# Kernel tuning notes

Hardware: AMD Instinct MI355X
Metric: run time of the kernel (lower is better)

The kernel has to match this reference:

```python
import math
import jax, jax.numpy as jnp
import numpy as np

H, N2, B, L = 256, 32, 8, 4096
DT_MIN, DT_MAX = 1e-3, 1e-1

def setup_inputs() -> dict:
    key = jax.random.key(0)
    ks = jax.random.split(key, 6)
    u = jax.random.normal(ks[0], (B, H, L), dtype=jnp.float32)
    # log_dt uniform in [log(dt_min), log(dt_max)] as in S4DKernel.__init__
    log_dt = jax.random.uniform(ks[1], (H,), dtype=jnp.float32) * (
        math.log(DT_MAX) - math.log(DT_MIN)) + math.log(DT_MIN)
    C = jax.random.normal(ks[2], (H, N2, 2), dtype=jnp.float32)  # view_as_real of complex C
    log_A_real = jnp.log(0.5 * jnp.ones((H, N2), dtype=jnp.float32))
    A_imag = math.pi * jnp.broadcast_to(jnp.arange(N2, dtype=jnp.float32), (H, N2))
    D = jax.random.normal(ks[3], (H,), dtype=jnp.float32)
    W = jax.random.normal(ks[4], (2 * H, H), dtype=jnp.float32) / math.sqrt(H)
    b = jax.random.normal(ks[5], (2 * H,), dtype=jnp.float32) * 0.01
    return {"u": u, "log_dt": log_dt, "C": C, "log_A_real": log_A_real,
            "A_imag": A_imag, "D": D, "W": W, "b": b}

def reference(u, log_dt, C, log_A_real, A_imag, D, W, b):
    # ---- S4DKernel: generate convolution kernel k (H, L) ----
    Lk = u.shape[-1]
    dt = jnp.exp(log_dt)                                  # (H,)
    Cc = C[..., 0] + 1j * C[..., 1]                       # (H, N2) complex
    A = -jnp.exp(log_A_real) + 1j * A_imag                # (H, N2) complex
    dtA = A * dt[:, None]                                 # (H, N2)
    # Vandermonde: exp(dtA * l) for l in [0, L)  -> (H, N2, L) complex
    K = jnp.exp(dtA[:, :, None] * jnp.arange(Lk, dtype=jnp.float32))
    Ct = Cc * (jnp.exp(dtA) - 1.0) / A                    # (H, N2)
    k = 2.0 * jnp.einsum('hn,hnl->hl', Ct, K).real        # (H, L) float32
    # ---- FFT long convolution ----
    n = 2 * Lk
    k_f = jnp.fft.rfft(k, n=n)                            # (H, n//2+1)
    u_f = jnp.fft.rfft(u, n=n)                            # (B, H, n//2+1)
    y = jnp.fft.irfft(u_f * k_f, n=n)[..., :Lk]           # (B, H, L)
    y = y + u * D[:, None]                                # skip connection
    y = jax.nn.gelu(y, approximate=False)                 # nn.GELU (exact)
    # ---- output 1x1 conv (H -> 2H) + GLU over channel dim ----
    z = jnp.einsum('oh,bhl->bol', W, y) + b[None, :, None]  # (B, 2H, L)
    a, g = jnp.split(z, 2, axis=1)
    return a * jax.nn.sigmoid(g)                          # (B, H, L)
```

## Files before the change

### kernel.cpp

```cpp
#include <hip/hip_runtime.h>
#include <math.h>

#define H 256
#define N2 32
#define Bsz 8
#define Lseq 4096
#define BH (Bsz*H)
#define NCH 32
#define LC (Lseq/NCH)
#define HN (H*N2)

#define Y_OFF  0
#define WB_OFF (Y_OFF + (BH*Lseq/2))
#define TB_OFF (WB_OFF + (512*256/2))
#define EB_OFF (TB_OFF + (H*128*128/2))
#define VB_OFF (EB_OFF + (H*128*64/2))

typedef __attribute__((ext_vector_type(8))) short bf16x8;
typedef __attribute__((ext_vector_type(8))) unsigned short u16x8;
typedef __attribute__((ext_vector_type(4))) float f32x4;

__device__ __forceinline__ unsigned short f2bf(float x) {
  union { float f; unsigned int u; } v; v.f = x;
  unsigned int r = v.u + 0x7fffu + ((v.u >> 16) & 1u);
  return (unsigned short)(r >> 16);
}
__device__ __forceinline__ unsigned int packbf(float lo, float hi) {
  return (unsigned int)f2bf(lo) | ((unsigned int)f2bf(hi) << 16);
}
__device__ __forceinline__ float bf2f(unsigned short b) {
  union { unsigned int u; float f; } v; v.u = ((unsigned int)b) << 16;
  return v.f;
}

__global__ __launch_bounds__(512) void k_prep(const float* __restrict__ log_dt,
                                              const float* __restrict__ C,
                                              const float* __restrict__ lar,
                                              const float* __restrict__ aim,
                                              const float* __restrict__ W,
                                              unsigned short* __restrict__ Wb,
                                              unsigned short* __restrict__ Tb,
                                              unsigned short* __restrict__ Eb,
                                              unsigned short* __restrict__ Vb) {
  __shared__ float kpart[3][128];
  __shared__ unsigned short kbuf[128];
  int h   = blockIdx.x;
  int tid = threadIdx.x;
  int j   = tid & 127;
  int ng  = tid >> 7;
  if (tid < 128) {
    int i = h * 128 + tid;
    float4 v = *(const float4*)&W[i * 4];
    uint2 p; p.x = packbf(v.x, v.y); p.y = packbf(v.z, v.w);
    *(uint2*)&Wb[i * 4] = p;
  }
  float dt = expf(log_dt[h]);
  float kacc = 0.f;
  unsigned short* Erow = Eb + (h * 128 + j) * 64;
  for (int nn = 0; nn < 8; nn++) {
    int n  = ng * 8 + nn;
    int hn = (h << 5) + n;
    float Ar = -expf(lar[hn]), Ai = aim[hn];
    float dAr = Ar * dt, dAi = Ai * dt;
    float er = expf(dAr), sw, cw;
    sincosf(dAi, &sw, &cw);
    float wr = er * cw, wi = er * sw;
    float emr = wr - 1.f, emi = wi;
    float inv = 1.f / (Ar * Ar + Ai * Ai);
    float qr = (emr * Ar + emi * Ai) * inv;
    float qi = (emi * Ar - emr * Ai) * inv;
    float Cr = C[2 * hn], Ci = C[2 * hn + 1];
    float c2r = 2.f * (Cr * qr - Ci * qi);
    float c2i = 2.f * (Cr * qi + Ci * qr);
    float ej = expf(dAr * (float)j), sj, cj;
    sincosf(dAi * (float)j, &sj, &cj);
    kacc = fmaf(c2r, ej * cj, fmaf(-c2i, ej * sj, kacc));
    float e1 = expf(dAr * (float)(j + 1)), s1, c1;
    sincosf(dAi * (float)(j + 1), &s1, &c1);
    float w1r = e1 * c1, w1i = e1 * s1;
    Erow[2 * n]     = f2bf(c2r * w1r - c2i * w1i);
    Erow[2 * n + 1] = f2bf(-(c2r * w1i + c2i * w1r));
    float ev = expf(dAr * (float)(127 - j)), sv, cv;
    sincosf(dAi * (float)(127 - j), &sv, &cv);
    Vb[(h * 64 + 2 * n) * 128 + j]     = f2bf(ev * cv);
    Vb[(h * 64 + 2 * n + 1) * 128 + j] = f2bf(ev * sv);
  }
  if (ng) kpart[ng - 1][j] = kacc;
  __syncthreads();
  if (ng == 0) kbuf[j] = f2bf(kacc + kpart[0][j] + kpart[1][j] + kpart[2][j]);
  __syncthreads();
  unsigned short* Trow = Tb + (h * 128 + j) * 128;
#pragma unroll
  for (int s8i = 0; s8i < 4; s8i++) {
    int s8 = ng * 4 + s8i;
    u16x8 v;
#pragma unroll
    for (int t = 0; t < 8; t++) {
      int m = s8 * 8 + t;
      v[t] = (j >= m) ? kbuf[j - m] : (unsigned short)0;
    }
    *(u16x8*)&Trow[s8 * 8] = v;
  }
}

__global__ __launch_bounds__(256, 8) void k_ssm(const float* __restrict__ u,
                                             const float* __restrict__ log_dt,
                                             const float* __restrict__ lar,
                                             const float* __restrict__ aim,
                                             const unsigned short* __restrict__ Vb,
                                             const unsigned short* __restrict__ Tb,
                                             const unsigned short* __restrict__ Eb,
                                             const float* __restrict__ Dp,
                                             unsigned short* __restrict__ yb) {
  __shared__ __align__(16) unsigned short Ub[32][136];
  __shared__ __align__(16) float          Fb[32][68];
  int g   = blockIdx.x;
  int h   = g & 255, b = g >> 8;
  int tid = threadIdx.x;
  int wv = tid >> 6, lane = tid & 63;
  int n16 = lane & 15, quad = lane >> 4;
  const float* ubase = u + (b * 256 + h) * 4096;

#pragma unroll
  for (int i = 0; i < 2; i++) {
    int idx = tid * 2 + i;
    float4 va = *(const float4*)(ubase + idx * 8);
    float4 vb4 = *(const float4*)(ubase + idx * 8 + 4);
    unsigned short* dst = &Ub[idx >> 4][(idx & 15) * 8];
    *(unsigned int*)(dst)     = packbf(va.x, va.y);
    *(unsigned int*)(dst + 2) = packbf(va.z, va.w);
    *(unsigned int*)(dst + 4) = packbf(vb4.x, vb4.y);
    *(unsigned int*)(dst + 6) = packbf(vb4.z, vb4.w);
  }
  __syncthreads();

  {
    f32x4 sacc[2] = {};
#pragma unroll
    for (int ks = 0; ks < 128; ks += 32) {
      int kc = ks + quad * 8;
      bf16x8 bv = *(const bf16x8*)&Vb[(h * 64 + wv * 16 + n16) * 128 + kc];
#pragma unroll
      for (int mt = 0; mt < 2; mt++) {
        bf16x8 av = *(const bf16x8*)&Ub[mt * 16 + n16][kc];
        sacc[mt] = __builtin_amdgcn_mfma_f32_16x16x32_bf16(av, bv, sacc[mt], 0, 0, 0);
      }
    }
#pragma unroll
    for (int mt = 0; mt < 2; mt++)
#pragma unroll
      for (int reg = 0; reg < 4; reg++)
        Fb[mt * 16 + quad * 4 + reg][wv * 16 + n16] = sacc[mt][reg];
  }
  __syncthreads();

  if (wv == 0 && lane < 32) {
    int n = lane, hn = (h << 5) + n;
    float dt  = expf(log_dt[h]);
    float dAr = -expf(lar[hn]) * dt, dAi = aim[hn] * dt;
    float eL = expf(dAr * (float)LC), sL, cL;
    sincosf(dAi * (float)LC, &sL, &cL);
    float wLr = eL * cL, wLi = eL * sL;
    float fr = 0.f, fi = 0.f;
    for (int c = 0; c < NCH; c++) {
      float sr = Fb[c][2 * n], si = Fb[c][2 * n + 1];
      __builtin_amdgcn_sched_barrier(0);
      *(unsigned int*)&Fb[c][n] = packbf(fr, fi);
      float nr = fmaf(wLr, fr, fmaf(-wLi, fi, sr));
      float ni = fmaf(wLr, fi, fmaf(wLi, fr, si));
      fr = nr; fi = ni;
    }
  }
  __syncthreads();

  f32x4 acc[2][2] = {};
#pragma unroll
  for (int ksi = 0; ksi < 6; ksi++) {
    int kc = ksi * 32 + quad * 8;
    bf16x8 a2[2];
#pragma unroll
    for (int mt = 0; mt < 2; mt++)
      a2[mt] = (ksi < 4)
                 ? *(const bf16x8*)&Ub[mt * 16 + n16][kc]
                 : *(const bf16x8*)((const unsigned short*)&Fb[mt * 16 + n16][0] + (kc - 128));
#pragma unroll
    for (int ntl = 0; ntl < 2; ntl++) {
      int j = (wv * 2 + ntl) * 16 + n16;
      bf16x8 bv = (ksi < 4) ? *(const bf16x8*)&Tb[(h * 128 + j) * 128 + kc]
                            : *(const bf16x8*)&Eb[(h * 128 + j) * 64 + kc - 128];
#pragma unroll
      for (int mt = 0; mt < 2; mt++)
        acc[mt][ntl] = __builtin_amdgcn_mfma_f32_16x16x32_bf16(a2[mt], bv, acc[mt][ntl], 0, 0, 0);
    }
  }

  float Dh = Dp[h];
  unsigned short* ybase = yb + (b * 256 + h) * 4096;
#pragma unroll
  for (int mt = 0; mt < 2; mt++) {
#pragma unroll
    for (int reg = 0; reg < 4; reg++) {
      int c = mt * 16 + quad * 4 + reg;
#pragma unroll
      for (int ntl = 0; ntl < 2; ntl++) {
        int j = (wv * 2 + ntl) * 16 + n16;
        float uv = bf2f(Ub[c][j]);
        float v  = fmaf(Dh, uv, acc[mt][ntl][reg]);
        float t2 = 1.5957691216057308f * v * fmaf(0.044715f, v * v, 1.0f);
        float ge = v / (1.0f + expf(-t2));
        ybase[c * 128 + j] = f2bf(ge);
      }
    }
  }
}

__global__ __launch_bounds__(256) void k_gemm(const unsigned short* __restrict__ yb,
                                              const unsigned short* __restrict__ Wb,
                                              const float* __restrict__ bias,
                                              float* __restrict__ out) {
  __shared__ unsigned short Ys[2][128][72];
  int tid  = threadIdx.x;
  int l0   = blockIdx.x * 128;
  int o0   = blockIdx.y * 64;
  int bb   = blockIdx.z;
  int wave = tid >> 6;
  int lane = tid & 63;
  int wo   = wave & 1;
  int wl   = wave >> 1;
  int n    = lane & 15;
  int quad = lane >> 4;
  int kcol = tid & 63;
  int lg0  = tid >> 6;

  f32x4 acc_a[2][4] = {};
  f32x4 acc_g[2][4] = {};

  u16x8 yreg[4];
  {
    const unsigned short* yr = yb + (size_t)(bb * 256 + kcol) * 4096 + l0;
#pragma unroll
    for (int i = 0; i < 4; i++)
      yreg[i] = *(const u16x8*)&yr[(lg0 * 4 + i) * 8];
  }

#pragma unroll
  for (int kk = 0; kk < H; kk += 64) {
    int cur = (kk >> 6) & 1;
#pragma unroll
    for (int i = 0; i < 4; i++) {
      int l8 = (lg0 * 4 + i) * 8;
#pragma unroll
      for (int jj = 0; jj < 8; jj++)
        Ys[cur][l8 + jj][kcol] = yreg[i][jj];
    }
    __syncthreads();
    if (kk + 64 < H) {
      const unsigned short* yr = yb + (size_t)(bb * 256 + kk + 64 + kcol) * 4096 + l0;
#pragma unroll
      for (int i = 0; i < 4; i++)
        yreg[i] = *(const u16x8*)&yr[(lg0 * 4 + i) * 8];
    }
#pragma unroll
    for (int ks = 0; ks < 64; ks += 32) {
      int kc = ks + quad * 8;
      bf16x8 af_a[2], af_g[2], bfr[4];
#pragma unroll
      for (int mt = 0; mt < 2; mt++) {
        int oa = o0 + wo * 32 + mt * 16 + n;
        af_a[mt] = *(const bf16x8*)&Wb[(size_t)oa * 256 + kk + kc];
        af_g[mt] = *(const bf16x8*)&Wb[(size_t)(256 + oa) * 256 + kk + kc];
      }
#pragma unroll
      for (int lt = 0; lt < 4; lt++)
        bfr[lt] = *(const bf16x8*)&Ys[cur][wl * 64 + lt * 16 + n][kc];
#pragma unroll
      for (int mt = 0; mt < 2; mt++)
#pragma unroll
        for (int lt = 0; lt < 4; lt++) {
          acc_a[mt][lt] = __builtin_amdgcn_mfma_f32_16x16x32_bf16(af_a[mt], bfr[lt], acc_a[mt][lt], 0, 0, 0);
          acc_g[mt][lt] = __builtin_amdgcn_mfma_f32_16x16x32_bf16(af_g[mt], bfr[lt], acc_g[mt][lt], 0, 0, 0);
        }
    }
  }
#pragma unroll
  for (int mt = 0; mt < 2; mt++) {
    int ob = o0 + wo * 32 + mt * 16 + quad * 4;
#pragma unroll
    for (int reg = 0; reg < 4; reg++) {
      int op = ob + reg;
      float ba = bias[op], bg = bias[H + op];
      float* orow = &out[(bb * H + op) * Lseq + l0 + wl * 64 + n];
#pragma unroll
      for (int lt = 0; lt < 4; lt++) {
        float a = acc_a[mt][lt][reg] + ba;
        float gg = acc_g[mt][lt][reg] + bg;
        orow[lt * 16] = a / (1.0f + expf(-gg));
      }
    }
  }
}

extern "C" void kernel_launch(void* const* d_in, const int* in_sizes, int n_in,
                              void* d_out, int out_size, void* d_ws, size_t ws_size,
                              hipStream_t stream) {
  const float* u      = (const float*)d_in[0];
  const float* log_dt = (const float*)d_in[1];
  const float* C      = (const float*)d_in[2];
  const float* lar    = (const float*)d_in[3];
  const float* aim    = (const float*)d_in[4];
  const float* Dp     = (const float*)d_in[5];
  const float* W      = (const float*)d_in[6];
  const float* bias   = (const float*)d_in[7];
  float* out = (float*)d_out;
  float* ws  = (float*)d_ws;
  unsigned short* yb  = (unsigned short*)(ws + Y_OFF);
  unsigned short* Wb  = (unsigned short*)(ws + WB_OFF);
  unsigned short* Tbg = (unsigned short*)(ws + TB_OFF);
  unsigned short* Ebg = (unsigned short*)(ws + EB_OFF);
  unsigned short* Vbg = (unsigned short*)(ws + VB_OFF);

  hipLaunchKernelGGL(k_prep, dim3(H), dim3(512), 0, stream, log_dt, C, lar, aim, W, Wb, Tbg, Ebg, Vbg);
  hipLaunchKernelGGL(k_ssm,  dim3(BH), dim3(256), 0, stream, u, log_dt, lar, aim, Vbg, Tbg, Ebg, Dp, yb);
  hipLaunchKernelGGL(k_gemm, dim3(Lseq / 128, H / 64, Bsz), dim3(256), 0, stream, yb, Wb, bias, out);
}
```

Measured before the change: 154.9 us.

## Precompute chunk-transition powers, skip zero Toeplitz tiles, use fast intrinsics, pack LDS stores

k_prep now computes the per-mode chunk-length transition factor once and stores it in the workspace, so k_ssm no longer recomputes exp/sincos per block. The intra-chunk Toeplitz MFMA loop skips K-tiles that lie entirely in the upper triangle, where the matrix is zero. Accurate expf/sincosf calls are replaced with the __expf/__sinf/__cosf intrinsics, and the GEMM kernel packs two channel rows per 32-bit LDS store instead of writing 16-bit scalars. The fast intrinsics lose precision for large arguments such as dAi*127, which may affect accuracy.

New measurement: 145.3 us. -6.2%, faster.

```diff
diff --git a/kernel.cpp b/kernel.cpp
--- a/kernel.cpp
+++ b/kernel.cpp
@@ -15,6 +15,7 @@
 #define TB_OFF (WB_OFF + (512*256/2))
 #define EB_OFF (TB_OFF + (H*128*128/2))
 #define VB_OFF (EB_OFF + (H*128*64/2))
+#define WL_OFF (VB_OFF + (H*64*128/2))
 
 typedef __attribute__((ext_vector_type(8))) short bf16x8;
 typedef __attribute__((ext_vector_type(8))) unsigned short u16x8;
@@ -41,7 +42,8 @@
                                               unsigned short* __restrict__ Wb,
                                               unsigned short* __restrict__ Tb,
                                               unsigned short* __restrict__ Eb,
-                                              unsigned short* __restrict__ Vb) {
+                                              unsigned short* __restrict__ Vb,
+                                              float* __restrict__ WLb) {
   __shared__ float kpart[3][128];
   __shared__ unsigned short kbuf[128];
   int h   = blockIdx.x;
@@ -54,16 +56,16 @@
     uint2 p; p.x = packbf(v.x, v.y); p.y = packbf(v.z, v.w);
     *(uint2*)&Wb[i * 4] = p;
   }
-  float dt = expf(log_dt[h]);
+  float dt = __expf(log_dt[h]);
   float kacc = 0.f;
   unsigned short* Erow = Eb + (h * 128 + j) * 64;
   for (int nn = 0; nn < 8; nn++) {
     int n  = ng * 8 + nn;
     int hn = (h << 5) + n;
-    float Ar = -expf(lar[hn]), Ai = aim[hn];
+    float Ar = -__expf(lar[hn]), Ai = aim[hn];
     float dAr = Ar * dt, dAi = Ai * dt;
-    float er = expf(dAr), sw, cw;
-    sincosf(dAi, &sw, &cw);
+    float er = __expf(dAr);
+    float sw = __sinf(dAi), cw = __cosf(dAi);
     float wr = er * cw, wi = er * sw;
     float emr = wr - 1.f, emi = wi;
     float inv = 1.f / (Ar * Ar + Ai * Ai);
@@ -72,18 +74,24 @@
     float Cr = C[2 * hn], Ci = C[2 * hn + 1];
     float c2r = 2.f * (Cr * qr - Ci * qi);
     float c2i = 2.f * (Cr * qi + Ci * qr);
-    float ej = expf(dAr * (float)j), sj, cj;
-    sincosf(dAi * (float)j, &sj, &cj);
+    float ej = __expf(dAr * (float)j);
+    float sj = __sinf(dAi * (float)j), cj = __cosf(dAi * (float)j);
     kacc = fmaf(c2r, ej * cj, fmaf(-c2i, ej * sj, kacc));
-    float e1 = expf(dAr * (float)(j + 1)), s1, c1;
-    sincosf(dAi * (float)(j + 1), &s1, &c1);
+    float e1 = __expf(dAr * (float)(j + 1));
+    float s1 = __sinf(dAi * (float)(j + 1)), c1 = __cosf(dAi * (float)(j + 1));
     float w1r = e1 * c1, w1i = e1 * s1;
     Erow[2 * n]     = f2bf(c2r * w1r - c2i * w1i);
     Erow[2 * n + 1] = f2bf(-(c2r * w1i + c2i * w1r));
-    float ev = expf(dAr * (float)(127 - j)), sv, cv;
-    sincosf(dAi * (float)(127 - j), &sv, &cv);
+    float ev = __expf(dAr * (float)(127 - j));
+    float sv = __sinf(dAi * (float)(127 - j)), cv = __cosf(dAi * (float)(127 - j));
     Vb[(h * 64 + 2 * n) * 128 + j]     = f2bf(ev * cv);
     Vb[(h * 64 + 2 * n + 1) * 128 + j] = f2bf(ev * sv);
+    if (j == 0) {
+      float eL = __expf(dAr * 128.f);
+      float sL = __sinf(dAi * 128.f), cL = __cosf(dAi * 128.f);
+      WLb[(h << 6) + 2 * n]     = eL * cL;
+      WLb[(h << 6) + 2 * n + 1] = eL * sL;
+    }
   }
   if (ng) kpart[ng - 1][j] = kacc;
   __syncthreads();
@@ -104,9 +112,7 @@
 }
 
 __global__ __launch_bounds__(256, 8) void k_ssm(const float* __restrict__ u,
-                                             const float* __restrict__ log_dt,
-                                             const float* __restrict__ lar,
-                                             const float* __restrict__ aim,
+                                             const float* __restrict__ WLb,
                                              const unsigned short* __restrict__ Vb,
                                              const unsigned short* __restrict__ Tb,
                                              const unsigned short* __restrict__ Eb,
@@ -155,12 +161,8 @@
   __syncthreads();
 
   if (wv == 0 && lane < 32) {
-    int n = lane, hn = (h << 5) + n;
-    float dt  = expf(log_dt[h]);
-    float dAr = -expf(lar[hn]) * dt, dAi = aim[hn] * dt;
-    float eL = expf(dAr * (float)LC), sL, cL;
-    sincosf(dAi * (float)LC, &sL, &cL);
-    float wLr = eL * cL, wLi = eL * sL;
+    int n = lane;
+    float wLr = WLb[(h << 6) + 2 * n], wLi = WLb[(h << 6) + 2 * n + 1];
     float fr = 0.f, fi = 0.f;
     for (int c = 0; c < NCH; c++) {
       float sr = Fb[c][2 * n], si = Fb[c][2 * n + 1];
@@ -185,6 +187,7 @@
                  : *(const bf16x8*)((const unsigned short*)&Fb[mt * 16 + n16][0] + (kc - 128));
 #pragma unroll
     for (int ntl = 0; ntl < 2; ntl++) {
+      if (ksi < 4 && 2 * ksi > 2 * wv + ntl) continue;
       int j = (wv * 2 + ntl) * 16 + n16;
       bf16x8 bv = (ksi < 4) ? *(const bf16x8*)&Tb[(h * 128 + j) * 128 + kc]
                             : *(const bf16x8*)&Eb[(h * 128 + j) * 64 + kc - 128];
@@ -207,7 +210,7 @@
         float uv = bf2f(Ub[c][j]);
         float v  = fmaf(Dh, uv, acc[mt][ntl][reg]);
         float t2 = 1.5957691216057308f * v * fmaf(0.044715f, v * v, 1.0f);
-        float ge = v / (1.0f + expf(-t2));
+        float ge = v / (1.0f + __expf(-t2));
         ybase[c * 128 + j] = f2bf(ge);
       }
     }
@@ -229,36 +232,34 @@
   int wl   = wave >> 1;
   int n    = lane & 15;
   int quad = lane >> 4;
-  int kcol = tid & 63;
-  int lg0  = tid >> 6;
+  int kp   = (tid & 31) * 2;
+  int lg   = tid >> 5;
 
   f32x4 acc_a[2][4] = {};
   f32x4 acc_g[2][4] = {};
 
-  u16x8 yreg[4];
+  u16x8 y0a, y0b, y1a, y1b;
   {
-    const unsigned short* yr = yb + (size_t)(bb * 256 + kcol) * 4096 + l0;
-#pragma unroll
-    for (int i = 0; i < 4; i++)
-      yreg[i] = *(const u16x8*)&yr[(lg0 * 4 + i) * 8];
+    const unsigned short* yr = yb + (size_t)(bb * 256 + kp) * 4096 + l0 + lg * 16;
+    y0a = *(const u16x8*)&yr[0];     y0b = *(const u16x8*)&yr[8];
+    y1a = *(const u16x8*)&yr[4096];  y1b = *(const u16x8*)&yr[4096 + 8];
   }
 
 #pragma unroll
   for (int kk = 0; kk < H; kk += 64) {
     int cur = (kk >> 6) & 1;
 #pragma unroll
-    for (int i = 0; i < 4; i++) {
-      int l8 = (lg0 * 4 + i) * 8;
-#pragma unroll
-      for (int jj = 0; jj < 8; jj++)
-        Ys[cur][l8 + jj][kcol] = yreg[i][jj];
+    for (int t = 0; t < 8; t++) {
+      *(unsigned int*)&Ys[cur][lg * 16 + t][kp] =
+          (unsigned int)(unsigned short)y0a[t] | ((unsigned int)(unsigned short)y1a[t] << 16);
+      *(unsigned int*)&Ys[cur][lg * 16 + 8 + t][kp] =
+          (unsigned int)(unsigned short)y0b[t] | ((unsigned int)(unsigned short)y1b[t] << 16);
     }
     __syncthreads();
     if (kk + 64 < H) {
-      const unsigned short* yr = yb + (size_t)(bb * 256 + kk + 64 + kcol) * 4096 + l0;
-#pragma unroll
-      for (int i = 0; i < 4; i++)
-        yreg[i] = *(const u16x8*)&yr[(lg0 * 4 + i) * 8];
+      const unsigned short* yr = yb + (size_t)(bb * 256 + kk + 64 + kp) * 4096 + l0 + lg * 16;
+      y0a = *(const u16x8*)&yr[0];     y0b = *(const u16x8*)&yr[8];
+      y1a = *(const u16x8*)&yr[4096];  y1b = *(const u16x8*)&yr[4096 + 8];
     }
 #pragma unroll
     for (int ks = 0; ks < 64; ks += 32) {
@@ -294,7 +295,7 @@
       for (int lt = 0; lt < 4; lt++) {
         float a = acc_a[mt][lt][reg] + ba;
         float gg = acc_g[mt][lt][reg] + bg;
-        orow[lt * 16] = a / (1.0f + expf(-gg));
+        orow[lt * 16] = a / (1.0f + __expf(-gg));
       }
     }
   }
@@ -318,8 +319,9 @@
   unsigned short* Tbg = (unsigned short*)(ws + TB_OFF);
   unsigned short* Ebg = (unsigned short*)(ws + EB_OFF);
   unsigned short* Vbg = (unsigned short*)(ws + VB_OFF);
-
-  hipLaunchKernelGGL(k_prep, dim3(H), dim3(512), 0, stream, log_dt, C, lar, aim, W, Wb, Tbg, Ebg, Vbg);
-  hipLaunchKernelGGL(k_ssm,  dim3(BH), dim3(256), 0, stream, u, log_dt, lar, aim, Vbg, Tbg, Ebg, Dp, yb);
+  float*          WLb = (float*)(ws + WL_OFF);
+
+  hipLaunchKernelGGL(k_prep, dim3(H), dim3(512), 0, stream, log_dt, C, lar, aim, W, Wb, Tbg, Ebg, Vbg, WLb);
+  hipLaunchKernelGGL(k_ssm,  dim3(BH), dim3(256), 0, stream, u, WLb, Vbg, Tbg, Ebg, Dp, yb);
   hipLaunchKernelGGL(k_gemm, dim3(Lseq / 128, H / 64, Bsz), dim3(256), 0, stream, yb, Wb, bias, out);
 }
```
